# Kernel tuning notes

Measured on AMD Instinct MI355X. Metric: run time of the kernel, lower is better.

Reference implementation:

```python
import jax, jax.numpy as jnp
import numpy as np

DIM = 1024
HEADS = 16
HEAD_DIM = DIM // HEADS
SCALE = HEAD_DIM ** -0.5


def setup_inputs() -> dict:
    key = jax.random.key(0)
    k1, k2, k3, k4 = jax.random.split(key, 4)
    x = jax.random.normal(k1, (2, 2048, DIM), dtype=jnp.float32)
    W_qkv = jax.random.normal(k2, (DIM, 3 * DIM), dtype=jnp.float32) * (DIM ** -0.5)
    W_out = jax.random.normal(k3, (DIM, DIM), dtype=jnp.float32) * (DIM ** -0.5)
    b_out = jax.random.normal(k4, (DIM,), dtype=jnp.float32) * 0.01
    return {"x": x, "W_qkv": W_qkv, "W_out": W_out, "b_out": b_out}


def reference(x, W_qkv, W_out, b_out):
    b, n, _ = x.shape
    qkv = x @ W_qkv  # [b, n, 3*dim]
    q, k, v = jnp.split(qkv, 3, axis=-1)
    # [b, n, dim] -> [b, h, n, d]
    def split_heads(t):
        return t.reshape(b, n, HEADS, HEAD_DIM).transpose(0, 2, 1, 3)
    q, k, v = split_heads(q), split_heads(k), split_heads(v)
    dots = jnp.einsum('bhid,bhjd->bhij', q, k) * SCALE
    attn = jax.nn.softmax(dots, axis=-1)
    out = jnp.einsum('bhij,bhjd->bhid', attn, v)
    out = out.transpose(0, 2, 1, 3).reshape(b, n, DIM)
    return out @ W_out + b_out
```

## Files before the change

kernel.cpp:

```cpp
#include <hip/hip_runtime.h>

#define DIM 1024
#define HEADS 16
#define HDIM 64
#define SEQ 2048
#define BATCH 2
#define MTOT (BATCH*SEQ)
#define ATT_SCALE 0.125f
#define LOG2E 1.4426950408889634f
#define QK_PRESCALE (ATT_SCALE * LOG2E)
#define FIXMAX 12.0f

typedef __attribute__((ext_vector_type(8))) short bf16x8;
typedef __attribute__((ext_vector_type(4))) short bf16x4;
typedef __attribute__((ext_vector_type(4))) float f32x4;
typedef __attribute__((ext_vector_type(4))) unsigned int u32x4;

__device__ __forceinline__ unsigned short f2bf(float f) {
  unsigned int u = __builtin_bit_cast(unsigned int, f);
  u += 0x7FFFu + ((u >> 16) & 1u);
  return (unsigned short)(u >> 16);
}

__device__ __forceinline__ unsigned int cvt_pk_bf16(float lo, float hi) {
  unsigned int r;
  asm("v_cvt_pk_bf16_f32 %0, %1, %2" : "=v"(r) : "v"(lo), "v"(hi));
  return r;
}

__device__ __forceinline__ void gl_lds16(const unsigned short* g, void* l) {
  __builtin_amdgcn_global_load_lds(
      (const __attribute__((address_space(1))) void*)g,
      (__attribute__((address_space(3))) void*)l, 16, 0, 0);
}

__global__ __launch_bounds__(256)
void cast_bf16_kernel(const float* __restrict__ src, unsigned short* __restrict__ dst, int n8) {
  int i = blockIdx.x * 256 + threadIdx.x;
  if (i >= n8) return;
  const float4* s = reinterpret_cast<const float4*>(src + (size_t)i * 8);
  float4 f0 = s[0], f1 = s[1];
  bf16x8 v;
  v[0] = (short)f2bf(f0.x); v[1] = (short)f2bf(f0.y);
  v[2] = (short)f2bf(f0.z); v[3] = (short)f2bf(f0.w);
  v[4] = (short)f2bf(f1.x); v[5] = (short)f2bf(f1.y);
  v[6] = (short)f2bf(f1.z); v[7] = (short)f2bf(f1.w);
  *reinterpret_cast<bf16x8*>(dst + (size_t)i * 8) = v;
}

__global__ __launch_bounds__(256)
void transpose_cast_kernel(const float* __restrict__ src, unsigned short* __restrict__ dst,
                           int R, int C) {
  __shared__ float tile[32][33];
  const int bx = blockIdx.x * 32;
  const int by = blockIdx.y * 32;
  const int tx = threadIdx.x, ty = threadIdx.y;
  #pragma unroll
  for (int i = 0; i < 32; i += 8)
    tile[ty + i][tx] = src[(size_t)(by + ty + i) * C + bx + tx];
  __syncthreads();
  #pragma unroll
  for (int i = 0; i < 32; i += 8)
    dst[(size_t)(bx + ty + i) * R + by + tx] = f2bf(tile[tx][ty + i]);
}

__global__ __launch_bounds__(256)
void transpose_v_kernel(const unsigned short* __restrict__ V, unsigned short* __restrict__ Vt) {
  __shared__ unsigned short tile[32][33];
  const int bh = blockIdx.z;
  const int n0 = blockIdx.x * 32, d0 = blockIdx.y * 32;
  const unsigned short* Vh = V + (size_t)bh * SEQ * HDIM;
  unsigned short* Vth = Vt + (size_t)bh * HDIM * SEQ;
  const int tx = threadIdx.x, ty = threadIdx.y;
  #pragma unroll
  for (int i = 0; i < 32; i += 8)
    tile[ty + i][tx] = Vh[(size_t)(n0 + ty + i) * HDIM + d0 + tx];
  __syncthreads();
  #pragma unroll
  for (int i = 0; i < 32; i += 8)
    Vth[(size_t)(d0 + ty + i) * SEQ + n0 + tx] = tile[tx][ty + i];
}

template<int EP, int BM>
__global__ __launch_bounds__(256)
void gemm_bf16_kernel(const unsigned short* __restrict__ A,
                      const unsigned short* __restrict__ Bt, const int K,
                      unsigned short* __restrict__ qbuf, unsigned short* __restrict__ kbuf,
                      unsigned short* __restrict__ vbuf,
                      float* __restrict__ outp, const float* __restrict__ bias) {
  constexpr int WM = BM / 32;
  __shared__ unsigned short As[2 * BM * 32];
  __shared__ unsigned short Bs[2 * 128 * 32];
  const int tid = threadIdx.x;
  const int lane = tid & 63, wid = tid >> 6;
  const int lq = lane & 15, lg = lane >> 4;
  const int wrow = wid >> 1, wcol = wid & 1;
  const int rowbase = blockIdx.y * BM;
  const int colbase = blockIdx.x * 128;
  const int sr = lane >> 2;
  const int sk = (lane & 3) * 8;

  f32x4 acc[WM][4];
  #pragma unroll
  for (int i = 0; i < WM; ++i)
    #pragma unroll
    for (int j = 0; j < 4; ++j) acc[i][j] = f32x4{0.f, 0.f, 0.f, 0.f};

  for (int kt = 0; kt < K; kt += 64) {
    #pragma unroll
    for (int i = 0; i < BM / 32; ++i) {
      const int c = wid * (BM / 32) + i;
      const int dh = c / (BM / 16);
      const int cc = c % (BM / 16);
      gl_lds16(A + (size_t)(rowbase + cc * 16 + sr) * K + kt + dh * 32 + sk, &As[c * 512]);
    }
    #pragma unroll
    for (int i = 0; i < 4; ++i) {
      const int c = wid * 4 + i;
      const int dh = c >> 3, cc = c & 7;
      gl_lds16(Bt + (size_t)(colbase + cc * 16 + sr) * K + kt + dh * 32 + sk, &Bs[c * 512]);
    }
    __syncthreads();

    bf16x8 af[2][WM], bfr[2][4];
    #pragma unroll
    for (int dh = 0; dh < 2; ++dh) {
      #pragma unroll
      for (int m4 = 0; m4 < WM; ++m4)
        af[dh][m4] = *reinterpret_cast<const bf16x8*>(
            &As[dh * BM * 32 + (wrow * (BM / 2) + m4 * 16 + lq) * 32 + lg * 8]);
      #pragma unroll
      for (int n4 = 0; n4 < 4; ++n4)
        bfr[dh][n4] = *reinterpret_cast<const bf16x8*>(
            &Bs[dh * 128 * 32 + (wcol * 64 + n4 * 16 + lq) * 32 + lg * 8]);
    }
    #pragma unroll
    for (int m4 = 0; m4 < WM; ++m4)
      #pragma unroll
      for (int n4 = 0; n4 < 4; ++n4) {
        acc[m4][n4] = __builtin_amdgcn_mfma_f32_16x16x32_bf16(af[0][m4], bfr[0][n4], acc[m4][n4], 0, 0, 0);
        acc[m4][n4] = __builtin_amdgcn_mfma_f32_16x16x32_bf16(af[1][m4], bfr[1][n4], acc[m4][n4], 0, 0, 0);
      }
    __syncthreads();
  }

  #pragma unroll
  for (int m4 = 0; m4 < WM; ++m4) {
    #pragma unroll
    for (int n4 = 0; n4 < 4; ++n4) {
      #pragma unroll
      for (int r = 0; r < 4; ++r) {
        int row = rowbase + wrow * (BM / 2) + m4 * 16 + lg * 4 + r;
        int col = colbase + wcol * 64 + n4 * 16 + lq;
        float val = acc[m4][n4][r];
        if (EP == 0) {
          int b = row >> 11, n = row & 2047;
          int which = col >> 10;
          int hc = col & 1023;
          int h = hc >> 6, d = hc & 63;
          size_t off = ((size_t)(b * HEADS + h) * SEQ + n) * HDIM + d;
          if (which == 0) qbuf[off] = f2bf(val * QK_PRESCALE);
          else if (which == 1) kbuf[off] = f2bf(val);
          else vbuf[off] = f2bf(val);
        } else {
          outp[(size_t)row * DIM + col] = val + bias[col];
        }
      }
    }
  }
}

__global__ __launch_bounds__(256)
void attn_kernel(const unsigned short* __restrict__ Q, const unsigned short* __restrict__ Kb,
                 const unsigned short* __restrict__ Vt, unsigned short* __restrict__ Obf) {
  __shared__ unsigned short Ks[2][64 * 64];
  __shared__ unsigned short Vs[2][64 * 64];
  const int bid = blockIdx.x;
  const int qblk = bid & 15, bh = bid >> 4;
  const int b = bh >> 4, h = bh & 15;
  const int tid = threadIdx.x;
  const int lane = tid & 63, wid = tid >> 6;
  const int lq = lane & 15, lg = lane >> 4;
  const int q0 = qblk * 128 + wid * 32;
  const unsigned short* Qh = Q + (size_t)bh * SEQ * HDIM;
  const unsigned short* Kh = Kb + (size_t)bh * SEQ * HDIM;
  const unsigned short* Vh = Vt + (size_t)bh * HDIM * SEQ;
  const int swz = (lq & 7) << 4;

  const int srow = tid >> 3;
  const int scol = (tid & 7) << 4;
  const int lw = srow * 128 + (scol ^ ((srow & 7) << 4));
  const char* gK = (const char*)Kh + srow * 128 + scol;
  const char* gV = (const char*)Vh + srow * 4096 + scol;

  bf16x8 qf[2][2];
  #pragma unroll
  for (int s = 0; s < 2; ++s)
    #pragma unroll
    for (int dh = 0; dh < 2; ++dh)
      qf[s][dh] = *reinterpret_cast<const bf16x8*>(Qh + (size_t)(q0 + s * 16 + lq) * HDIM + dh * 32 + lg * 8);

  f32x4 acc[2][4];
  #pragma unroll
  for (int s = 0; s < 2; ++s)
    #pragma unroll
    for (int dc = 0; dc < 4; ++dc) acc[s][dc] = f32x4{0.f, 0.f, 0.f, 0.f};
  float lsum[2] = {0.f, 0.f};

  bf16x8 rK0, rK1, rV0, rV1;
  rK0 = *reinterpret_cast<const bf16x8*>(gK);
  rK1 = *reinterpret_cast<const bf16x8*>(gK + 4096);
  rV0 = *reinterpret_cast<const bf16x8*>(gV);
  rV1 = *reinterpret_cast<const bf16x8*>(gV + 32 * 4096);
  {
    char* kb = (char*)&Ks[0][0];
    char* vb = (char*)&Vs[0][0];
    *reinterpret_cast<bf16x8*>(kb + lw) = rK0;
    *reinterpret_cast<bf16x8*>(kb + lw + 4096) = rK1;
    *reinterpret_cast<bf16x8*>(vb + lw) = rV0;
    *reinterpret_cast<bf16x8*>(vb + lw + 4096) = rV1;
  }
  __syncthreads();

  const int NT = SEQ / 64;
  for (int it = 0; it < NT; ++it) {
    const int cur = it & 1;
    const bool pre = (it + 1 < NT);
    if (pre) {
      const int kt = (it + 1) * 64;
      rK0 = *reinterpret_cast<const bf16x8*>(gK + kt * 128);
      rK1 = *reinterpret_cast<const bf16x8*>(gK + kt * 128 + 4096);
      rV0 = *reinterpret_cast<const bf16x8*>(gV + kt * 2);
      rV1 = *reinterpret_cast<const bf16x8*>(gV + kt * 2 + 32 * 4096);
    }

    const char* KsB = (const char*)&Ks[cur][0];
    const char* VsB = (const char*)&Vs[cur][0];

    bf16x8 kf[4][2];
    #pragma unroll
    for (int t = 0; t < 4; ++t)
      #pragma unroll
      for (int dh = 0; dh < 2; ++dh)
        kf[t][dh] = *reinterpret_cast<const bf16x8*>(
            KsB + (t * 16 + lq) * 128 + ((dh * 64 + lg * 16) ^ swz));

    f32x4 st[2][4];
    #pragma unroll
    for (int s = 0; s < 2; ++s)
      #pragma unroll
      for (int t = 0; t < 4; ++t) {
        f32x4 z = f32x4{-FIXMAX, -FIXMAX, -FIXMAX, -FIXMAX};
        z = __builtin_amdgcn_mfma_f32_16x16x32_bf16(kf[t][0], qf[s][0], z, 0, 0, 0);
        st[s][t] = __builtin_amdgcn_mfma_f32_16x16x32_bf16(kf[t][1], qf[s][1], z, 0, 0, 0);
      }

    #pragma unroll
    for (int s = 0; s < 2; ++s)
      #pragma unroll
      for (int t = 0; t < 4; ++t)
        #pragma unroll
        for (int r = 0; r < 4; ++r) {
          st[s][t][r] = __builtin_amdgcn_exp2f(st[s][t][r]);
          lsum[s] += st[s][t][r];
        }

    #pragma unroll
    for (int hh = 0; hh < 2; ++hh) {
      bf16x8 pf[2];
      #pragma unroll
      for (int s = 0; s < 2; ++s) {
        unsigned int a0 = cvt_pk_bf16(st[s][2 * hh][0], st[s][2 * hh][1]);
        unsigned int a1 = cvt_pk_bf16(st[s][2 * hh][2], st[s][2 * hh][3]);
        unsigned int c0 = cvt_pk_bf16(st[s][2 * hh + 1][0], st[s][2 * hh + 1][1]);
        unsigned int c1 = cvt_pk_bf16(st[s][2 * hh + 1][2], st[s][2 * hh + 1][3]);
        asm volatile("v_permlane32_swap_b32 %0, %1" : "+v"(a0), "+v"(c0));
        asm volatile("v_permlane16_swap_b32 %0, %1" : "+v"(a0), "+v"(c0));
        asm volatile("v_permlane32_swap_b32 %0, %1" : "+v"(a1), "+v"(c1));
        asm volatile("v_permlane16_swap_b32 %0, %1" : "+v"(a1), "+v"(c1));
        u32x4 w;
        w[0] = a0;
        w[1] = a1;
        w[2] = c0;
        w[3] = c1;
        pf[s] = __builtin_bit_cast(bf16x8, w);
      }
      #pragma unroll
      for (int dc = 0; dc < 4; ++dc) {
        bf16x8 vf = *reinterpret_cast<const bf16x8*>(
            VsB + (dc * 16 + lq) * 128 + ((hh * 64 + lg * 16) ^ swz));
        acc[0][dc] = __builtin_amdgcn_mfma_f32_16x16x32_bf16(vf, pf[0], acc[0][dc], 0, 0, 0);
        acc[1][dc] = __builtin_amdgcn_mfma_f32_16x16x32_bf16(vf, pf[1], acc[1][dc], 0, 0, 0);
      }
    }

    if (pre) {
      char* kb = (char*)&Ks[cur ^ 1][0];
      char* vb = (char*)&Vs[cur ^ 1][0];
      *reinterpret_cast<bf16x8*>(kb + lw) = rK0;
      *reinterpret_cast<bf16x8*>(kb + lw + 4096) = rK1;
      *reinterpret_cast<bf16x8*>(vb + lw) = rV0;
      *reinterpret_cast<bf16x8*>(vb + lw + 4096) = rV1;
    }
    __syncthreads();
  }

  #pragma unroll
  for (int s = 0; s < 2; ++s) {
    float ls = lsum[s];
    ls += __shfl_xor(ls, 16);
    ls += __shfl_xor(ls, 32);
    float inv = 1.f / ls;
    const int qg = q0 + s * 16 + lq;
    unsigned short* orow = Obf + (size_t)(b * SEQ + qg) * DIM + h * HDIM + lg * 4;
    #pragma unroll
    for (int dc = 0; dc < 4; ++dc) {
      bf16x4 o;
      o[0] = (short)f2bf(acc[s][dc][0] * inv);
      o[1] = (short)f2bf(acc[s][dc][1] * inv);
      o[2] = (short)f2bf(acc[s][dc][2] * inv);
      o[3] = (short)f2bf(acc[s][dc][3] * inv);
      *reinterpret_cast<bf16x4*>(orow + dc * 16) = o;
    }
  }
}

extern "C" void kernel_launch(void* const* d_in, const int* in_sizes, int n_in,
                              void* d_out, int out_size, void* d_ws, size_t ws_size,
                              hipStream_t stream) {
  const float* x     = (const float*)d_in[0];
  const float* Wqkv  = (const float*)d_in[1];
  const float* Wout  = (const float*)d_in[2];
  const float* bout  = (const float*)d_in[3];
  float* out = (float*)d_out;

  char* ws = (char*)d_ws;
  unsigned short* WqkvT = (unsigned short*)ws; ws += (size_t)3 * DIM * DIM * 2;
  unsigned short* WoutT = (unsigned short*)ws; ws += (size_t)DIM * DIM * 2;
  unsigned short* Qb    = (unsigned short*)ws; ws += (size_t)32 * SEQ * HDIM * 2;
  unsigned short* Kbuf  = (unsigned short*)ws; ws += (size_t)32 * SEQ * HDIM * 2;
  unsigned short* Vbuf  = (unsigned short*)ws; ws += (size_t)32 * SEQ * HDIM * 2;
  unsigned short* Vtb   = (unsigned short*)ws; ws += (size_t)32 * SEQ * HDIM * 2;
  unsigned short* xbf   = (unsigned short*)ws; ws += (size_t)MTOT * DIM * 2;
  unsigned short* Obf   = (unsigned short*)ws; ws += (size_t)MTOT * DIM * 2;

  dim3 b32x8(32, 8);
  cast_bf16_kernel<<<dim3((MTOT * DIM / 8) / 256), 256, 0, stream>>>(x, xbf, MTOT * DIM / 8);
  transpose_cast_kernel<<<dim3((3 * DIM) / 32, DIM / 32), b32x8, 0, stream>>>(Wqkv, WqkvT, DIM, 3 * DIM);
  transpose_cast_kernel<<<dim3(DIM / 32, DIM / 32), b32x8, 0, stream>>>(Wout, WoutT, DIM, DIM);
  gemm_bf16_kernel<0, 128><<<dim3((3 * DIM) / 128, MTOT / 128), 256, 0, stream>>>(
      xbf, WqkvT, DIM, Qb, Kbuf, Vbuf, nullptr, nullptr);
  transpose_v_kernel<<<dim3(SEQ / 32, HDIM / 32, 32), b32x8, 0, stream>>>(Vbuf, Vtb);
  attn_kernel<<<dim3(512), 256, 0, stream>>>(Qb, Kbuf, Vtb, Obf);
  gemm_bf16_kernel<1, 64><<<dim3(DIM / 128, MTOT / 64), 256, 0, stream>>>(
      Obf, WoutT, DIM, nullptr, nullptr, nullptr, out, bout);
}
```

Baseline: 191.9 us.

## Add XCD-aware block swizzle and widen attention KV tile to 128

```diff
diff --git a/kernel.cpp b/kernel.cpp
--- a/kernel.cpp
+++ b/kernel.cpp
@@ -26,6 +26,10 @@
   unsigned int r;
   asm("v_cvt_pk_bf16_f32 %0, %1, %2" : "=v"(r) : "v"(lo), "v"(hi));
   return r;
+}
+
+__device__ __forceinline__ int xcd_swz(int bid, int nwg) {
+  return (bid & 7) * (nwg >> 3) + (bid >> 3);
 }
 
 __device__ __forceinline__ void gl_lds16(const unsigned short* g, void* l) {
@@ -84,19 +88,20 @@
 template<int EP, int BM>
 __global__ __launch_bounds__(256)
 void gemm_bf16_kernel(const unsigned short* __restrict__ A,
-                      const unsigned short* __restrict__ Bt, const int K,
+                      const unsigned short* __restrict__ Bt, const int K, const int gx,
                       unsigned short* __restrict__ qbuf, unsigned short* __restrict__ kbuf,
                       unsigned short* __restrict__ vbuf,
                       float* __restrict__ outp, const float* __restrict__ bias) {
   constexpr int WM = BM / 32;
   __shared__ unsigned short As[2 * BM * 32];
   __shared__ unsigned short Bs[2 * 128 * 32];
+  const int wg = xcd_swz(blockIdx.x, gridDim.x);
   const int tid = threadIdx.x;
   const int lane = tid & 63, wid = tid >> 6;
   const int lq = lane & 15, lg = lane >> 4;
   const int wrow = wid >> 1, wcol = wid & 1;
-  const int rowbase = blockIdx.y * BM;
-  const int colbase = blockIdx.x * 128;
+  const int rowbase = (wg / gx) * BM;
+  const int colbase = (wg % gx) * 128;
   const int sr = lane >> 2;
   const int sk = (lane & 3) * 8;
 
@@ -173,10 +178,10 @@
 __global__ __launch_bounds__(256)
 void attn_kernel(const unsigned short* __restrict__ Q, const unsigned short* __restrict__ Kb,
                  const unsigned short* __restrict__ Vt, unsigned short* __restrict__ Obf) {
-  __shared__ unsigned short Ks[2][64 * 64];
-  __shared__ unsigned short Vs[2][64 * 64];
-  const int bid = blockIdx.x;
-  const int qblk = bid & 15, bh = bid >> 4;
+  __shared__ unsigned short Ks[2][128 * 64];
+  __shared__ unsigned short Vs[2][64 * 128];
+  const int wg = xcd_swz(blockIdx.x, gridDim.x);
+  const int qblk = wg & 15, bh = wg >> 4;
   const int b = bh >> 4, h = bh & 15;
   const int tid = threadIdx.x;
   const int lane = tid & 63, wid = tid >> 6;
@@ -189,9 +194,12 @@
 
   const int srow = tid >> 3;
   const int scol = (tid & 7) << 4;
-  const int lw = srow * 128 + (scol ^ ((srow & 7) << 4));
+  const int lwK = srow * 128 + (scol ^ ((srow & 7) << 4));
   const char* gK = (const char*)Kh + srow * 128 + scol;
-  const char* gV = (const char*)Vh + srow * 4096 + scol;
+  const int vrow = tid >> 4;
+  const int vcol = (tid & 15) << 4;
+  const int lwV = vrow * 256 + (vcol ^ ((vrow & 7) << 4));
+  const char* gV = (const char*)Vh + vrow * 4096 + vcol;
 
   bf16x8 qf[2][2];
   #pragma unroll
@@ -207,100 +215,107 @@
     for (int dc = 0; dc < 4; ++dc) acc[s][dc] = f32x4{0.f, 0.f, 0.f, 0.f};
   float lsum[2] = {0.f, 0.f};
 
-  bf16x8 rK0, rK1, rV0, rV1;
-  rK0 = *reinterpret_cast<const bf16x8*>(gK);
-  rK1 = *reinterpret_cast<const bf16x8*>(gK + 4096);
-  rV0 = *reinterpret_cast<const bf16x8*>(gV);
-  rV1 = *reinterpret_cast<const bf16x8*>(gV + 32 * 4096);
+  bf16x8 rK[4], rV[4];
+  #pragma unroll
+  for (int j = 0; j < 4; ++j) {
+    rK[j] = *reinterpret_cast<const bf16x8*>(gK + j * 4096);
+    rV[j] = *reinterpret_cast<const bf16x8*>(gV + j * 65536);
+  }
   {
     char* kb = (char*)&Ks[0][0];
     char* vb = (char*)&Vs[0][0];
-    *reinterpret_cast<bf16x8*>(kb + lw) = rK0;
-    *reinterpret_cast<bf16x8*>(kb + lw + 4096) = rK1;
-    *reinterpret_cast<bf16x8*>(vb + lw) = rV0;
-    *reinterpret_cast<bf16x8*>(vb + lw + 4096) = rV1;
+    #pragma unroll
+    for (int j = 0; j < 4; ++j) {
+      *reinterpret_cast<bf16x8*>(kb + lwK + j * 4096) = rK[j];
+      *reinterpret_cast<bf16x8*>(vb + lwV + j * 4096) = rV[j];
+    }
   }
   __syncthreads();
 
-  const int NT = SEQ / 64;
+  const int NT = SEQ / 128;
   for (int it = 0; it < NT; ++it) {
     const int cur = it & 1;
     const bool pre = (it + 1 < NT);
     if (pre) {
-      const int kt = (it + 1) * 64;
-      rK0 = *reinterpret_cast<const bf16x8*>(gK + kt * 128);
-      rK1 = *reinterpret_cast<const bf16x8*>(gK + kt * 128 + 4096);
-      rV0 = *reinterpret_cast<const bf16x8*>(gV + kt * 2);
-      rV1 = *reinterpret_cast<const bf16x8*>(gV + kt * 2 + 32 * 4096);
+      const int kt = (it + 1) * 128;
+      #pragma unroll
+      for (int j = 0; j < 4; ++j) {
+        rK[j] = *reinterpret_cast<const bf16x8*>(gK + (size_t)kt * 128 + j * 4096);
+        rV[j] = *reinterpret_cast<const bf16x8*>(gV + (size_t)kt * 2 + j * 65536);
+      }
     }
 
     const char* KsB = (const char*)&Ks[cur][0];
     const char* VsB = (const char*)&Vs[cur][0];
 
-    bf16x8 kf[4][2];
-    #pragma unroll
-    for (int t = 0; t < 4; ++t)
-      #pragma unroll
-      for (int dh = 0; dh < 2; ++dh)
-        kf[t][dh] = *reinterpret_cast<const bf16x8*>(
-            KsB + (t * 16 + lq) * 128 + ((dh * 64 + lg * 16) ^ swz));
-
-    f32x4 st[2][4];
-    #pragma unroll
-    for (int s = 0; s < 2; ++s)
-      #pragma unroll
-      for (int t = 0; t < 4; ++t) {
-        f32x4 z = f32x4{-FIXMAX, -FIXMAX, -FIXMAX, -FIXMAX};
-        z = __builtin_amdgcn_mfma_f32_16x16x32_bf16(kf[t][0], qf[s][0], z, 0, 0, 0);
-        st[s][t] = __builtin_amdgcn_mfma_f32_16x16x32_bf16(kf[t][1], qf[s][1], z, 0, 0, 0);
-      }
-
-    #pragma unroll
-    for (int s = 0; s < 2; ++s)
+    #pragma unroll
+    for (int h1 = 0; h1 < 2; ++h1) {
+      bf16x8 kf[4][2];
       #pragma unroll
       for (int t = 0; t < 4; ++t)
         #pragma unroll
-        for (int r = 0; r < 4; ++r) {
-          st[s][t][r] = __builtin_amdgcn_exp2f(st[s][t][r]);
-          lsum[s] += st[s][t][r];
+        for (int dh = 0; dh < 2; ++dh)
+          kf[t][dh] = *reinterpret_cast<const bf16x8*>(
+              KsB + (h1 * 64 + t * 16 + lq) * 128 + ((dh * 64 + lg * 16) ^ swz));
+
+      f32x4 st[2][4];
+      #pragma unroll
+      for (int s = 0; s < 2; ++s)
+        #pragma unroll
+        for (int t = 0; t < 4; ++t) {
+          f32x4 z = f32x4{-FIXMAX, -FIXMAX, -FIXMAX, -FIXMAX};
+          z = __builtin_amdgcn_mfma_f32_16x16x32_bf16(kf[t][0], qf[s][0], z, 0, 0, 0);
+          st[s][t] = __builtin_amdgcn_mfma_f32_16x16x32_bf16(kf[t][1], qf[s][1], z, 0, 0, 0);
         }
 
-    #pragma unroll
-    for (int hh = 0; hh < 2; ++hh) {
-      bf16x8 pf[2];
-      #pragma unroll
-      for (int s = 0; s < 2; ++s) {
-        unsigned int a0 = cvt_pk_bf16(st[s][2 * hh][0], st[s][2 * hh][1]);
-        unsigned int a1 = cvt_pk_bf16(st[s][2 * hh][2], st[s][2 * hh][3]);
-        unsigned int c0 = cvt_pk_bf16(st[s][2 * hh + 1][0], st[s][2 * hh + 1][1]);
-        unsigned int c1 = cvt_pk_bf16(st[s][2 * hh + 1][2], st[s][2 * hh + 1][3]);
-        asm volatile("v_permlane32_swap_b32 %0, %1" : "+v"(a0), "+v"(c0));
-        asm volatile("v_permlane16_swap_b32 %0, %1" : "+v"(a0), "+v"(c0));
-        asm volatile("v_permlane32_swap_b32 %0, %1" : "+v"(a1), "+v"(c1));
-        asm volatile("v_permlane16_swap_b32 %0, %1" : "+v"(a1), "+v"(c1));
-        u32x4 w;
-        w[0] = a0;
-        w[1] = a1;
-        w[2] = c0;
-        w[3] = c1;
-        pf[s] = __builtin_bit_cast(bf16x8, w);
-      }
-      #pragma unroll
-      for (int dc = 0; dc < 4; ++dc) {
-        bf16x8 vf = *reinterpret_cast<const bf16x8*>(
-            VsB + (dc * 16 + lq) * 128 + ((hh * 64 + lg * 16) ^ swz));
-        acc[0][dc] = __builtin_amdgcn_mfma_f32_16x16x32_bf16(vf, pf[0], acc[0][dc], 0, 0, 0);
-        acc[1][dc] = __builtin_amdgcn_mfma_f32_16x16x32_bf16(vf, pf[1], acc[1][dc], 0, 0, 0);
+      #pragma unroll
+      for (int s = 0; s < 2; ++s)
+        #pragma unroll
+        for (int t = 0; t < 4; ++t)
+          #pragma unroll
+          for (int r = 0; r < 4; ++r) {
+            st[s][t][r] = __builtin_amdgcn_exp2f(st[s][t][r]);
+            lsum[s] += st[s][t][r];
+          }
+
+      #pragma unroll
+      for (int hh = 0; hh < 2; ++hh) {
+        bf16x8 pf[2];
+        #pragma unroll
+        for (int s = 0; s < 2; ++s) {
+          unsigned int a0 = cvt_pk_bf16(st[s][2 * hh][0], st[s][2 * hh][1]);
+          unsigned int a1 = cvt_pk_bf16(st[s][2 * hh][2], st[s][2 * hh][3]);
+          unsigned int c0 = cvt_pk_bf16(st[s][2 * hh + 1][0], st[s][2 * hh + 1][1]);
+          unsigned int c1 = cvt_pk_bf16(st[s][2 * hh + 1][2], st[s][2 * hh + 1][3]);
+          asm volatile("v_permlane32_swap_b32 %0, %1" : "+v"(a0), "+v"(c0));
+          asm volatile("v_permlane16_swap_b32 %0, %1" : "+v"(a0), "+v"(c0));
+          asm volatile("v_permlane32_swap_b32 %0, %1" : "+v"(a1), "+v"(c1));
+          asm volatile("v_permlane16_swap_b32 %0, %1" : "+v"(a1), "+v"(c1));
+          u32x4 w;
+          w[0] = a0;
+          w[1] = a1;
+          w[2] = c0;
+          w[3] = c1;
+          pf[s] = __builtin_bit_cast(bf16x8, w);
+        }
+        #pragma unroll
+        for (int dc = 0; dc < 4; ++dc) {
+          bf16x8 vf = *reinterpret_cast<const bf16x8*>(
+              VsB + (dc * 16 + lq) * 256 + ((h1 * 128 + hh * 64 + lg * 16) ^ swz));
+          acc[0][dc] = __builtin_amdgcn_mfma_f32_16x16x32_bf16(vf, pf[0], acc[0][dc], 0, 0, 0);
+          acc[1][dc] = __builtin_amdgcn_mfma_f32_16x16x32_bf16(vf, pf[1], acc[1][dc], 0, 0, 0);
+        }
       }
     }
 
     if (pre) {
       char* kb = (char*)&Ks[cur ^ 1][0];
       char* vb = (char*)&Vs[cur ^ 1][0];
-      *reinterpret_cast<bf16x8*>(kb + lw) = rK0;
-      *reinterpret_cast<bf16x8*>(kb + lw + 4096) = rK1;
-      *reinterpret_cast<bf16x8*>(vb + lw) = rV0;
-      *reinterpret_cast<bf16x8*>(vb + lw + 4096) = rV1;
+      #pragma unroll
+      for (int j = 0; j < 4; ++j) {
+        *reinterpret_cast<bf16x8*>(kb + lwK + j * 4096) = rK[j];
+        *reinterpret_cast<bf16x8*>(vb + lwV + j * 4096) = rV[j];
+      }
     }
     __syncthreads();
   }
@@ -348,10 +363,10 @@
   cast_bf16_kernel<<<dim3((MTOT * DIM / 8) / 256), 256, 0, stream>>>(x, xbf, MTOT * DIM / 8);
   transpose_cast_kernel<<<dim3((3 * DIM) / 32, DIM / 32), b32x8, 0, stream>>>(Wqkv, WqkvT, DIM, 3 * DIM);
   transpose_cast_kernel<<<dim3(DIM / 32, DIM / 32), b32x8, 0, stream>>>(Wout, WoutT, DIM, DIM);
-  gemm_bf16_kernel<0, 128><<<dim3((3 * DIM) / 128, MTOT / 128), 256, 0, stream>>>(
-      xbf, WqkvT, DIM, Qb, Kbuf, Vbuf, nullptr, nullptr);
+  gemm_bf16_kernel<0, 128><<<dim3(((3 * DIM) / 128) * (MTOT / 128)), 256, 0, stream>>>(
+      xbf, WqkvT, DIM, (3 * DIM) / 128, Qb, Kbuf, Vbuf, nullptr, nullptr);
   transpose_v_kernel<<<dim3(SEQ / 32, HDIM / 32, 32), b32x8, 0, stream>>>(Vbuf, Vtb);
   attn_kernel<<<dim3(512), 256, 0, stream>>>(Qb, Kbuf, Vtb, Obf);
-  gemm_bf16_kernel<1, 64><<<dim3(DIM / 128, MTOT / 64), 256, 0, stream>>>(
-      Obf, WoutT, DIM, nullptr, nullptr, nullptr, out, bout);
-}
+  gemm_bf16_kernel<1, 64><<<dim3((DIM / 128) * (MTOT / 64)), 256, 0, stream>>>(
+      Obf, WoutT, DIM, DIM / 128, nullptr, nullptr, nullptr, out, bout);
+}
```

Measured after the change: 182.6 us. -4.8%, faster.
